# Kernel tuning notes

Hardware: AMD Instinct MI355X
Metric: run time of the kernel (lower is better)

Reference implementation:

```python
import jax, jax.numpy as jnp
import numpy as np

B, T, S, H = 8, 256, 256, 512

def setup_inputs() -> dict:
    key = jax.random.key(0)
    k1, k2, k3, k4, k5, k6 = jax.random.split(key, 6)
    query = jax.random.normal(k1, (B, T, H), dtype=jnp.float32)
    encoder_outputs = jax.random.normal(k2, (B, S, H), dtype=jnp.float32)
    # lengths in [1, S] so every row has at least one valid source position
    src_lengths = jax.random.randint(k3, (B,), 1, S + 1, dtype=jnp.int64)
    scale = 1.0 / np.sqrt(H)
    W_h = jax.random.normal(k4, (H, H), dtype=jnp.float32) * scale  # nn.Linear weight (out, in)
    W_s = jax.random.normal(k5, (H, H), dtype=jnp.float32) * scale
    v = jax.random.normal(k6, (H,), dtype=jnp.float32) * scale     # nn.Linear(H,1) weight squeezed
    return {"query": query, "encoder_outputs": encoder_outputs,
            "src_lengths": src_lengths, "W_h": W_h, "W_s": W_s, "v": v}

def reference(query, encoder_outputs, src_lengths, W_h, W_s, v):
    # Linear without bias: y = x @ W^T
    enc_f = jnp.einsum('bsh,oh->bso', encoder_outputs, W_h)   # (B,S,H)
    qry_f = jnp.einsum('bth,oh->bto', query, W_s)             # (B,T,H)
    # additive score: v^T tanh(enc_f + qry_f), broadcast over (T,S)
    scores = jnp.einsum('btsh,h->bts',
                        jnp.tanh(enc_f[:, None, :, :] + qry_f[:, :, None, :]), v)  # (B,T,S)
    mask = jnp.arange(S)[None, :] >= src_lengths[:, None]      # (B,S) True = pad
    scores = jnp.where(mask[:, None, :], -jnp.inf, scores)
    attn_weights = jax.nn.softmax(scores, axis=-1)             # (B,T,S)
    attn_out = jnp.einsum('bts,bsh->bth', attn_weights, encoder_outputs)
    return attn_out
```

## Files before the change

### kernel.cpp

```cpp
#include <hip/hip_runtime.h>
#include <cstddef>
#include <math.h>

#define BD 8
#define TD 256
#define SD 256
#define HD 512
#define K2F 2.885390081777927f

#define EXP2(x) __builtin_amdgcn_exp2f(x)
#define RCP(x)  __builtin_amdgcn_rcpf(x)

typedef __attribute__((ext_vector_type(8))) _Float16 half8;
typedef __attribute__((ext_vector_type(4))) _Float16 half4;
typedef __attribute__((ext_vector_type(4))) float float4v;

__device__ __forceinline__ float exp2_sat(float x) {
    return EXP2(fminf(fmaxf(x, -80.0f), 80.0f));
}

#define LSTR 40

__global__ __launch_bounds__(1024) void projK(
    const float* __restrict__ enc, const float* __restrict__ qry,
    const float* __restrict__ Wh,  const float* __restrict__ Ws,
    float* __restrict__ encT, float* __restrict__ encS, float* __restrict__ qryf)
{
    __shared__ float smem[2560];

    const int bid = blockIdx.x;
    const int tid = threadIdx.x;
    const int l  = tid & 63;
    const int w  = tid >> 6;
    const int rf = l & 15;
    const int q  = l >> 4;

    _Float16* LA = (_Float16*)smem;
    _Float16* LB = (_Float16*)(smem + 1280);

    const int x  = bid & 7;
    const int k  = bid >> 3;
    const bool isq = k >= 32;
    const int kk = k & 31;
    const int my = (isq ? 32 : 0) + x * 4 + (kk & 3);
    const int n0 = (kk >> 2) * 64;
    const int m0 = my * 64;

    const bool stagesA = (tid < 512);
    const int srow = (tid >> 3) & 63;
    const int scol = (tid & 7) * 4;
    const float* Sbase = stagesA
        ? (isq ? qry + (size_t)(m0 - 2048 + srow) * HD
               : enc + (size_t)(m0 + srow) * HD) + scol
        : (isq ? Ws : Wh) + (size_t)(n0 + srow) * HD + scol;
    _Float16* Ldst = (stagesA ? LA : LB) + srow * LSTR + scol;

    const int mi = (w & 3) * 16;
    const int ni = (w >> 2) * 16;

    float4v acc = {0, 0, 0, 0};

    float4 a0 = *(const float4*)(Sbase);

    for (int ks = 0; ks < 16; ++ks) {
        if (ks) __syncthreads();
        {
            half4 ha;
            ha[0]=(_Float16)a0.x; ha[1]=(_Float16)a0.y; ha[2]=(_Float16)a0.z; ha[3]=(_Float16)a0.w;
            *(half4*)Ldst = ha;
        }
        __syncthreads();
        if (ks + 1 < 16) a0 = *(const float4*)(Sbase + (ks + 1) * 32);
        half8 ah = *(const half8*)&LA[(mi + rf) * LSTR + q * 8];
        half8 bh = *(const half8*)&LB[(ni + rf) * LSTR + q * 8];
        acc = __builtin_amdgcn_mfma_f32_16x16x32_f16(ah, bh, acc, 0, 0, 0);
    }

    if (!isq) {
        const int b  = m0 >> 8;
        const int sb = (m0 & 255) + mi + q * 4;
        const int h  = n0 + ni + rf;
        float e0 = exp2_sat(acc[0]*K2F), e1 = exp2_sat(acc[1]*K2F);
        float e2 = exp2_sat(acc[2]*K2F), e3 = exp2_sat(acc[3]*K2F);
        *(float4*)(encT + (size_t)b * HD * SD + (size_t)h * SD + sb) =
            make_float4(e0, e1, e2, e3);
        float* es = encS + ((size_t)b * SD + sb) * HD + h;
        es[0 * HD] = e0; es[1 * HD] = e1; es[2 * HD] = e2; es[3 * HD] = e3;
    } else {
        const int mrow = (m0 - 2048) + mi + q * 4;
        #pragma unroll
        for (int r = 0; r < 4; ++r)
            qryf[(size_t)(mrow + r) * HD + n0 + ni + rf] = exp2_sat(acc[r] * K2F);
    }
}

__global__ __launch_bounds__(1024, 1) void scoreS(
    const float* __restrict__ encS, const float* __restrict__ qryf,
    const float* __restrict__ v, const int* __restrict__ lens,
    float* __restrict__ part2)
{
    __shared__ float qls[4096];
    __shared__ float red[16 * 576];

    const int bid = blockIdx.x;
    const int tid = threadIdx.x;
    const int b    = bid >> 6;
    const int rest = bid & 63;
    const int toct = rest >> 1;
    const int sh   = rest & 1;
    const int t0   = toct * 8;
    const int len  = lens[b];

    if (sh * 128 >= len) return;

    {
        const float* qf = qryf + ((size_t)b * TD + t0) * HD;
        const int i = tid * 4;
        *(float4*)&qls[i] = *(const float4*)(qf + (i >> 9) * HD + (i & 511));
    }
    __syncthreads();

    const int l = tid & 63;
    const int w = tid >> 6;
    float* rb = red + w * 576;

    float4 qreg[2][8];
    #pragma unroll
    for (int i = 0; i < 2; ++i)
        #pragma unroll
        for (int t = 0; t < 8; ++t)
            qreg[i][t] = *(const float4*)&qls[t * 512 + i * 256 + 4 * l];
    float4 vreg[2];
    #pragma unroll
    for (int i = 0; i < 2; ++i)
        vreg[i] = *(const float4*)(v + i * 256 + 4 * l);

    const int tsel = l & 7;
    const int ck   = l >> 3;

    for (int k = 0; k < 8; ++k) {
        const int s = sh * 128 + k * 16 + w;
        if (s >= len) break;

        const float* eb = encS + ((size_t)b * SD + s) * HD;
        float a[8];
        #pragma unroll
        for (int t = 0; t < 8; ++t) a[t] = 0.0f;

        #pragma unroll
        for (int i = 0; i < 2; ++i) {
            float4 e4 = *(const float4*)(eb + i * 256 + 4 * l);
            float4 v4 = vreg[i];
            #pragma unroll
            for (int t = 0; t < 8; ++t) {
                float4 q4 = qreg[i][t];
                float p;
                p = fmaf(e4.x, q4.x, 1.0f); a[t] = fmaf(v4.x, RCP(p), a[t]);
                p = fmaf(e4.y, q4.y, 1.0f); a[t] = fmaf(v4.y, RCP(p), a[t]);
                p = fmaf(e4.z, q4.z, 1.0f); a[t] = fmaf(v4.z, RCP(p), a[t]);
                p = fmaf(e4.w, q4.w, 1.0f); a[t] = fmaf(v4.w, RCP(p), a[t]);
            }
        }

        *(float4*)&rb[l * 9 + 0] = make_float4(a[0], a[1], a[2], a[3]);
        *(float4*)&rb[l * 9 + 4] = make_float4(a[4], a[5], a[6], a[7]);
        float part = 0.0f;
        #pragma unroll
        for (int i = 0; i < 8; ++i)
            part += rb[(ck * 8 + i) * 9 + tsel];
        part += __shfl_xor(part, 8);
        part += __shfl_xor(part, 16);
        part += __shfl_xor(part, 32);
        if (l < 8)
            part2[((size_t)b * TD + t0 + l) * SD + s] = part;
    }
}

__global__ __launch_bounds__(512) void attn3K(
    const float* __restrict__ enc, const float* __restrict__ part2,
    const int* __restrict__ lens, float* __restrict__ out)
{
    __shared__ float avred[8192];
    __shared__ float wls[4 * SD];

    const int bid = blockIdx.x;
    const int tid = threadIdx.x;
    const int b   = bid & 7;
    const int t0  = (bid >> 3) * 4;
    const int w   = tid >> 6;
    const int l   = tid & 63;

    if (w < 4) {
        const int t = w;
        const int s0 = l * 4;
        float4 h0 = *(const float4*)(part2 + ((size_t)b * TD + t0 + t) * SD + s0);
        float p[4] = {h0.x, h0.y, h0.z, h0.w};
        const int len = lens[b];
        float sc[4];
        #pragma unroll
        for (int c = 0; c < 4; ++c)
            sc[c] = (s0 + c < len) ? -2.0f * p[c] : -INFINITY;
        float mx = fmaxf(fmaxf(sc[0], sc[1]), fmaxf(sc[2], sc[3]));
        #pragma unroll
        for (int off = 32; off; off >>= 1) mx = fmaxf(mx, __shfl_xor(mx, off));
        float ex[4]; float sum = 0.0f;
        #pragma unroll
        for (int c = 0; c < 4; ++c) { ex[c] = __expf(sc[c] - mx); sum += ex[c]; }
        #pragma unroll
        for (int off = 32; off; off >>= 1) sum += __shfl_xor(sum, off);
        const float inv = RCP(sum);
        *(float4*)&wls[t * SD + s0] = make_float4(ex[0]*inv, ex[1]*inv, ex[2]*inv, ex[3]*inv);
    }
    __syncthreads();

    const int g  = tid >> 7;
    const int h4 = (tid & 127) * 4;
    {
        const float* eb = enc + (size_t)b * SD * HD + h4;
        float4 o[4] = {{0,0,0,0},{0,0,0,0},{0,0,0,0},{0,0,0,0}};
        #pragma unroll 2
        for (int ss = 0; ss < 64; ++ss) {
            const int s = g * 64 + ss;
            float4 evv = *(const float4*)(eb + (size_t)s * HD);
            float wt[4];
            #pragma unroll
            for (int t = 0; t < 4; ++t) wt[t] = wls[t * SD + s];
            #pragma unroll
            for (int t = 0; t < 4; ++t) {
                o[t].x = fmaf(wt[t], evv.x, o[t].x);
                o[t].y = fmaf(wt[t], evv.y, o[t].y);
                o[t].z = fmaf(wt[t], evv.z, o[t].z);
                o[t].w = fmaf(wt[t], evv.w, o[t].w);
            }
        }
        #pragma unroll
        for (int t = 0; t < 4; ++t)
            *(float4*)&avred[(size_t)(g * 4 + t) * 512 + h4] = o[t];
    }
    __syncthreads();
    {
        const int t  = tid >> 7;
        const int hh = (tid & 127) * 4;
        float4 r = {0, 0, 0, 0};
        #pragma unroll
        for (int gg = 0; gg < 4; ++gg) {
            float4 x = *(const float4*)&avred[(size_t)(gg * 4 + t) * 512 + hh];
            r.x += x.x; r.y += x.y; r.z += x.z; r.w += x.w;
        }
        *(float4*)(out + ((size_t)b * TD + t0 + t) * HD + hh) = r;
    }
}

__global__ __launch_bounds__(1024) void attnK(
    const float* __restrict__ enc, const float* __restrict__ encT,
    const float* __restrict__ qryf, const float* __restrict__ v,
    const int* __restrict__ lens, float* __restrict__ out)
{
    __shared__ float smem[14336];

    const int bid = blockIdx.x;
    const int tid = threadIdx.x;
    const int b   = bid & 7;
    const int t0  = (bid >> 3) * 8;
    const int l = tid & 63;
    const int w = tid >> 6;

    float* qls = smem;
    float* pls = smem + 4096;
    float* wls = smem + 12288;

    {
        const float* qf = qryf + ((size_t)b * TD + t0) * HD;
        const int j = tid & 511;
        #pragma unroll
        for (int t = (tid >> 9); t < 8; t += 2)
            qls[t * 512 + j] = qf[t * HD + j];
    }
    __syncthreads();

    float a[8][4];
    #pragma unroll
    for (int t = 0; t < 8; ++t)
        #pragma unroll
        for (int c = 0; c < 4; ++c) a[t][c] = 0.0f;
    {
        const int jbase = w * 32;
        const float* ep = encT + (size_t)b * HD * SD + (size_t)jbase * SD + l * 4;
        #pragma unroll 4
        for (int jj = 0; jj < 32; ++jj) {
            float4 e = *(const float4*)(ep + (size_t)jj * SD);
            float vj = v[jbase + jj];
            float qv[8];
            #pragma unroll
            for (int t = 0; t < 8; ++t) qv[t] = qls[t * 512 + jbase + jj];
            float ev[4] = {e.x, e.y, e.z, e.w};
            #pragma unroll
            for (int t = 0; t < 8; ++t)
                #pragma unroll
                for (int c = 0; c < 4; ++c) {
                    float p = fmaf(ev[c], qv[t], 1.0f);
                    a[t][c] = fmaf(vj, RCP(p), a[t][c]);
                }
        }
    }
    if (w < 4) {
        #pragma unroll
        for (int t = 0; t < 8; ++t)
            *(float4*)&pls[(w * 8 + t) * 256 + l * 4] =
                make_float4(a[t][0], a[t][1], a[t][2], a[t][3]);
    }
    __syncthreads();
    if (w >= 4 && w < 8) {
        #pragma unroll
        for (int t = 0; t < 8; ++t) {
            float4 c4 = *(const float4*)&pls[((w - 4) * 8 + t) * 256 + l * 4];
            c4.x += a[t][0]; c4.y += a[t][1]; c4.z += a[t][2]; c4.w += a[t][3];
            *(float4*)&pls[((w - 4) * 8 + t) * 256 + l * 4] = c4;
        }
    }
    __syncthreads();
    if (w >= 8 && w < 12) {
        #pragma unroll
        for (int t = 0; t < 8; ++t) {
            float4 c4 = *(const float4*)&pls[((w - 8) * 8 + t) * 256 + l * 4];
            c4.x += a[t][0]; c4.y += a[t][1]; c4.z += a[t][2]; c4.w += a[t][3];
            *(float4*)&pls[((w - 8) * 8 + t) * 256 + l * 4] = c4;
        }
    }
    __syncthreads();
    if (w >= 12) {
        #pragma unroll
        for (int t = 0; t < 8; ++t) {
            float4 c4 = *(const float4*)&pls[((w - 12) * 8 + t) * 256 + l * 4];
            c4.x += a[t][0]; c4.y += a[t][1]; c4.z += a[t][2]; c4.w += a[t][3];
            *(float4*)&pls[((w - 12) * 8 + t) * 256 + l * 4] = c4;
        }
    }
    __syncthreads();

    if (w < 8) {
        const int t = w;
        float p[4] = {0, 0, 0, 0};
        #pragma unroll
        for (int g = 0; g < 4; ++g) {
            float4 pp = *(const float4*)&pls[(g * 8 + t) * 256 + l * 4];
            p[0] += pp.x; p[1] += pp.y; p[2] += pp.z; p[3] += pp.w;
        }
        const int len = lens[b];
        const int s0 = l * 4;
        float sc[4];
        #pragma unroll
        for (int c = 0; c < 4; ++c)
            sc[c] = (s0 + c < len) ? -2.0f * p[c] : -INFINITY;
        float mx = fmaxf(fmaxf(sc[0], sc[1]), fmaxf(sc[2], sc[3]));
        #pragma unroll
        for (int off = 32; off; off >>= 1) mx = fmaxf(mx, __shfl_xor(mx, off));
        float ex[4]; float sum = 0.0f;
        #pragma unroll
        for (int c = 0; c < 4; ++c) { ex[c] = __expf(sc[c] - mx); sum += ex[c]; }
        #pragma unroll
        for (int off = 32; off; off >>= 1) sum += __shfl_xor(sum, off);
        const float inv = RCP(sum);
        *(float4*)&wls[t * SD + s0] = make_float4(ex[0]*inv, ex[1]*inv, ex[2]*inv, ex[3]*inv);
    }
    __syncthreads();

    const int sg = tid >> 7;
    const int h4 = (tid & 127) * 4;
    float* avred = pls;
    float4 o[8];
    #pragma unroll
    for (int t = 0; t < 8; ++t) o[t] = make_float4(0.f, 0.f, 0.f, 0.f);
    {
        const float* eb = enc + (size_t)b * SD * HD + h4;
        #pragma unroll 2
        for (int ss = 0; ss < 32; ++ss) {
            const int s = sg * 32 + ss;
            float4 evv = *(const float4*)(eb + (size_t)s * HD);
            float wt[8];
            #pragma unroll
            for (int t = 0; t < 8; ++t) wt[t] = wls[t * SD + s];
            #pragma unroll
            for (int t = 0; t < 8; ++t) {
                o[t].x = fmaf(wt[t], evv.x, o[t].x);
                o[t].y = fmaf(wt[t], evv.y, o[t].y);
                o[t].z = fmaf(wt[t], evv.z, o[t].z);
                o[t].w = fmaf(wt[t], evv.w, o[t].w);
            }
        }
    }
    if (sg < 2) {
        #pragma unroll
        for (int t = 0; t < 8; ++t)
            *(float4*)&avred[(size_t)(sg * 8 + t) * 512 + h4] = o[t];
    }
    __syncthreads();
    if (sg >= 2 && sg < 4) {
        #pragma unroll
        for (int t = 0; t < 8; ++t) {
            float4 c4 = *(const float4*)&avred[(size_t)((sg - 2) * 8 + t) * 512 + h4];
            c4.x += o[t].x; c4.y += o[t].y; c4.z += o[t].z; c4.w += o[t].w;
            *(float4*)&avred[(size_t)((sg - 2) * 8 + t) * 512 + h4] = c4;
        }
    }
    __syncthreads();
    if (sg >= 4 && sg < 6) {
        #pragma unroll
        for (int t = 0; t < 8; ++t) {
            float4 c4 = *(const float4*)&avred[(size_t)((sg - 4) * 8 + t) * 512 + h4];
            c4.x += o[t].x; c4.y += o[t].y; c4.z += o[t].z; c4.w += o[t].w;
            *(float4*)&avred[(size_t)((sg - 4) * 8 + t) * 512 + h4] = c4;
        }
    }
    __syncthreads();
    if (sg >= 6) {
        #pragma unroll
        for (int t = 0; t < 8; ++t) {
            float4 c4 = *(const float4*)&avred[(size_t)((sg - 6) * 8 + t) * 512 + h4];
            c4.x += o[t].x; c4.y += o[t].y; c4.z += o[t].z; c4.w += o[t].w;
            *(float4*)&avred[(size_t)((sg - 6) * 8 + t) * 512 + h4] = c4;
        }
    }
    __syncthreads();

    {
        const int t  = tid >> 7;
        const int hh = (tid & 127) * 4;
        float4 x0 = *(const float4*)&avred[(size_t)(0 * 8 + t) * 512 + hh];
        float4 x1 = *(const float4*)&avred[(size_t)(1 * 8 + t) * 512 + hh];
        float4 r = make_float4(x0.x + x1.x, x0.y + x1.y, x0.z + x1.z, x0.w + x1.w);
        *(float4*)(out + ((size_t)b * TD + t0 + t) * HD + hh) = r;
    }
}

extern "C" void kernel_launch(void* const* d_in, const int* in_sizes, int n_in,
                              void* d_out, int out_size, void* d_ws, size_t ws_size,
                              hipStream_t stream) {
    const float* query = (const float*)d_in[0];
    const float* enc   = (const float*)d_in[1];
    const int*   lens  = (const int*)d_in[2];
    const float* W_h   = (const float*)d_in[3];
    const float* W_s   = (const float*)d_in[4];
    const float* v     = (const float*)d_in[5];
    float* out = (float*)d_out;

    char* ws = (char*)d_ws;
    float* encT  = (float*)(ws);
    float* qryf  = (float*)(ws + ((size_t)4 << 20));
    float* encS  = (float*)(ws + ((size_t)8 << 20));
    float* part2 = (float*)(ws + ((size_t)12 << 20));

    projK<<<dim3(512), dim3(1024), 0, stream>>>(enc, query, W_h, W_s, encT, encS, qryf);

    bool use_s = (ws_size >= ((size_t)14 << 20));
    hipFuncAttributes fa{};
    if (use_s &&
        hipFuncGetAttributes(&fa, (const void*)scoreS) == hipSuccess &&
        fa.localSizeBytes > 0) {
        use_s = false;
    }

    if (use_s) {
        scoreS<<<dim3(512), dim3(1024), 0, stream>>>(encS, qryf, v, lens, part2);
        attn3K<<<dim3(512), dim3(512),  0, stream>>>(enc, part2, lens, out);
    } else {
        attnK<<<dim3(256), dim3(1024), 0, stream>>>(enc, encT, qryf, v, lens, out);
    }
}
```

Before: 123.9 us.

## Fuse score and attention-output kernels into one block per 8 queries

```diff
diff --git a/kernel.cpp b/kernel.cpp
--- a/kernel.cpp
+++ b/kernel.cpp
@@ -94,24 +94,27 @@
     }
 }
 
-__global__ __launch_bounds__(1024, 1) void scoreS(
-    const float* __restrict__ encS, const float* __restrict__ qryf,
-    const float* __restrict__ v, const int* __restrict__ lens,
-    float* __restrict__ part2)
+__global__ __launch_bounds__(1024, 1) void attnF(
+    const float* __restrict__ enc, const float* __restrict__ encS,
+    const float* __restrict__ qryf, const float* __restrict__ v,
+    const int* __restrict__ lens, float* __restrict__ out)
 {
-    __shared__ float qls[4096];
-    __shared__ float red[16 * 576];
+    __shared__ float smem[15392];
+
+    float* qls   = smem;
+    float* wq    = smem;
+    float* red   = smem + 4096;
+    float* avred = smem + 4096;
+    float* ssc   = smem + 13312;
 
     const int bid = blockIdx.x;
     const int tid = threadIdx.x;
-    const int b    = bid >> 6;
-    const int rest = bid & 63;
-    const int toct = rest >> 1;
-    const int sh   = rest & 1;
+    const int b    = bid >> 5;
+    const int toct = bid & 31;
     const int t0   = toct * 8;
     const int len  = lens[b];
-
-    if (sh * 128 >= len) return;
+    const int l = tid & 63;
+    const int w = tid >> 6;
 
     {
         const float* qf = qryf + ((size_t)b * TD + t0) * HD;
@@ -119,10 +122,6 @@
         *(float4*)&qls[i] = *(const float4*)(qf + (i >> 9) * HD + (i & 511));
     }
     __syncthreads();
-
-    const int l = tid & 63;
-    const int w = tid >> 6;
-    float* rb = red + w * 576;
 
     float4 qreg[2][8];
     #pragma unroll
@@ -137,9 +136,10 @@
 
     const int tsel = l & 7;
     const int ck   = l >> 3;
-
-    for (int k = 0; k < 8; ++k) {
-        const int s = sh * 128 + k * 16 + w;
+    float* rb = red + w * 576;
+
+    for (int k = 0; k < 16; ++k) {
+        const int s = k * 16 + w;
         if (s >= len) break;
 
         const float* eb = encS + ((size_t)b * SD + s) * HD;
@@ -172,30 +172,18 @@
         part += __shfl_xor(part, 16);
         part += __shfl_xor(part, 32);
         if (l < 8)
-            part2[((size_t)b * TD + t0 + l) * SD + s] = part;
-    }
-}
-
-__global__ __launch_bounds__(512) void attn3K(
-    const float* __restrict__ enc, const float* __restrict__ part2,
-    const int* __restrict__ lens, float* __restrict__ out)
-{
-    __shared__ float avred[8192];
-    __shared__ float wls[4 * SD];
-
-    const int bid = blockIdx.x;
-    const int tid = threadIdx.x;
-    const int b   = bid & 7;
-    const int t0  = (bid >> 3) * 4;
-    const int w   = tid >> 6;
-    const int l   = tid & 63;
-
-    if (w < 4) {
+            ssc[l * 260 + s] = part;
+    }
+    __syncthreads();
+
+    if (w < 8) {
         const int t = w;
         const int s0 = l * 4;
-        float4 h0 = *(const float4*)(part2 + ((size_t)b * TD + t0 + t) * SD + s0);
-        float p[4] = {h0.x, h0.y, h0.z, h0.w};
-        const int len = lens[b];
+        float p0 = ssc[t * 260 + s0 + 0];
+        float p1 = ssc[t * 260 + s0 + 1];
+        float p2 = ssc[t * 260 + s0 + 2];
+        float p3 = ssc[t * 260 + s0 + 3];
+        float p[4] = {p0, p1, p2, p3};
         float sc[4];
         #pragma unroll
         for (int c = 0; c < 4; ++c)
@@ -209,44 +197,78 @@
         #pragma unroll
         for (int off = 32; off; off >>= 1) sum += __shfl_xor(sum, off);
         const float inv = RCP(sum);
-        *(float4*)&wls[t * SD + s0] = make_float4(ex[0]*inv, ex[1]*inv, ex[2]*inv, ex[3]*inv);
-    }
-    __syncthreads();
-
-    const int g  = tid >> 7;
+        #pragma unroll
+        for (int c = 0; c < 4; ++c)
+            wq[(s0 + c) * 12 + t] = ex[c] * inv;
+    }
+    __syncthreads();
+
+    const int sg = tid >> 7;
     const int h4 = (tid & 127) * 4;
+    float4 o[8];
+    #pragma unroll
+    for (int t = 0; t < 8; ++t) o[t] = make_float4(0.f, 0.f, 0.f, 0.f);
     {
         const float* eb = enc + (size_t)b * SD * HD + h4;
-        float4 o[4] = {{0,0,0,0},{0,0,0,0},{0,0,0,0},{0,0,0,0}};
         #pragma unroll 2
-        for (int ss = 0; ss < 64; ++ss) {
-            const int s = g * 64 + ss;
+        for (int ss = 0; ss < 32; ++ss) {
+            const int s = sg * 32 + ss;
+            if (s >= len) break;
             float4 evv = *(const float4*)(eb + (size_t)s * HD);
-            float wt[4];
-            #pragma unroll
-            for (int t = 0; t < 4; ++t) wt[t] = wls[t * SD + s];
-            #pragma unroll
-            for (int t = 0; t < 4; ++t) {
+            float4 w0 = *(const float4*)&wq[s * 12 + 0];
+            float4 w1 = *(const float4*)&wq[s * 12 + 4];
+            float wt[8] = {w0.x, w0.y, w0.z, w0.w, w1.x, w1.y, w1.z, w1.w};
+            #pragma unroll
+            for (int t = 0; t < 8; ++t) {
                 o[t].x = fmaf(wt[t], evv.x, o[t].x);
                 o[t].y = fmaf(wt[t], evv.y, o[t].y);
                 o[t].z = fmaf(wt[t], evv.z, o[t].z);
                 o[t].w = fmaf(wt[t], evv.w, o[t].w);
             }
         }
-        #pragma unroll
-        for (int t = 0; t < 4; ++t)
-            *(float4*)&avred[(size_t)(g * 4 + t) * 512 + h4] = o[t];
-    }
-    __syncthreads();
+    }
+    __syncthreads();
+
+    if (sg < 2) {
+        #pragma unroll
+        for (int t = 0; t < 8; ++t)
+            *(float4*)&avred[(size_t)(sg * 8 + t) * 512 + h4] = o[t];
+    }
+    __syncthreads();
+    if (sg >= 2 && sg < 4) {
+        #pragma unroll
+        for (int t = 0; t < 8; ++t) {
+            float4 c4 = *(const float4*)&avred[(size_t)((sg - 2) * 8 + t) * 512 + h4];
+            c4.x += o[t].x; c4.y += o[t].y; c4.z += o[t].z; c4.w += o[t].w;
+            *(float4*)&avred[(size_t)((sg - 2) * 8 + t) * 512 + h4] = c4;
+        }
+    }
+    __syncthreads();
+    if (sg >= 4 && sg < 6) {
+        #pragma unroll
+        for (int t = 0; t < 8; ++t) {
+            float4 c4 = *(const float4*)&avred[(size_t)((sg - 4) * 8 + t) * 512 + h4];
+            c4.x += o[t].x; c4.y += o[t].y; c4.z += o[t].z; c4.w += o[t].w;
+            *(float4*)&avred[(size_t)((sg - 4) * 8 + t) * 512 + h4] = c4;
+        }
+    }
+    __syncthreads();
+    if (sg >= 6) {
+        #pragma unroll
+        for (int t = 0; t < 8; ++t) {
+            float4 c4 = *(const float4*)&avred[(size_t)((sg - 6) * 8 + t) * 512 + h4];
+            c4.x += o[t].x; c4.y += o[t].y; c4.z += o[t].z; c4.w += o[t].w;
+            *(float4*)&avred[(size_t)((sg - 6) * 8 + t) * 512 + h4] = c4;
+        }
+    }
+    __syncthreads();
+
     {
         const int t  = tid >> 7;
         const int hh = (tid & 127) * 4;
-        float4 r = {0, 0, 0, 0};
-        #pragma unroll
-        for (int gg = 0; gg < 4; ++gg) {
-            float4 x = *(const float4*)&avred[(size_t)(gg * 4 + t) * 512 + hh];
-            r.x += x.x; r.y += x.y; r.z += x.z; r.w += x.w;
-        }
+        float4 x0 = *(const float4*)&avred[(size_t)(0 * 8 + t) * 512 + hh];
+        float4 x1 = *(const float4*)&avred[(size_t)(1 * 8 + t) * 512 + hh];
+        float4 r = make_float4(x0.x + x1.x, x0.y + x1.y, x0.z + x1.z, x0.w + x1.w);
         *(float4*)(out + ((size_t)b * TD + t0 + t) * HD + hh) = r;
     }
 }
@@ -448,21 +470,19 @@
     float* encT  = (float*)(ws);
     float* qryf  = (float*)(ws + ((size_t)4 << 20));
     float* encS  = (float*)(ws + ((size_t)8 << 20));
-    float* part2 = (float*)(ws + ((size_t)12 << 20));
 
     projK<<<dim3(512), dim3(1024), 0, stream>>>(enc, query, W_h, W_s, encT, encS, qryf);
 
-    bool use_s = (ws_size >= ((size_t)14 << 20));
+    bool use_f = (ws_size >= ((size_t)12 << 20));
     hipFuncAttributes fa{};
-    if (use_s &&
-        hipFuncGetAttributes(&fa, (const void*)scoreS) == hipSuccess &&
+    if (use_f &&
+        hipFuncGetAttributes(&fa, (const void*)attnF) == hipSuccess &&
         fa.localSizeBytes > 0) {
-        use_s = false;
-    }
-
-    if (use_s) {
-        scoreS<<<dim3(512), dim3(1024), 0, stream>>>(encS, qryf, v, lens, part2);
-        attn3K<<<dim3(512), dim3(512),  0, stream>>>(enc, part2, lens, out);
+        use_f = false;
+    }
+
+    if (use_f) {
+        attnF<<<dim3(256), dim3(1024), 0, stream>>>(enc, encS, qryf, v, lens, out);
     } else {
         attnK<<<dim3(256), dim3(1024), 0, stream>>>(enc, encT, qryf, v, lens, out);
     }
```

Result: faster. 120.6 us (-2.7%).
